# Kernel tuning notes

Hardware: AMD Instinct MI355X
Metric: run time of the kernel (lower is better)

Reference implementation:

```python
import jax, jax.numpy as jnp
import numpy as np

E, I, D = 8, 2816, 1024   # num_experts, intermediate_size, dim
T, A = 1024, 2            # tokens, top-k experts per token


def setup_inputs() -> dict:
    key = jax.random.key(0)
    k1, k2, k3, k4, k5 = jax.random.split(key, 5)
    x = jax.random.normal(k1, (T, D), dtype=jnp.float32)
    expert_indices = jax.random.randint(k2, (T, A), 0, E, dtype=jnp.int64)
    scale = 0.02
    w1 = jax.random.normal(k3, (E, I, D), dtype=jnp.float32) * scale
    w2 = jax.random.normal(k4, (E, D, I), dtype=jnp.float32) * scale
    w3 = jax.random.normal(k5, (E, I, D), dtype=jnp.float32) * scale
    return {"x": x, "w1": w1, "w2": w2, "w3": w3, "expert_indices": expert_indices}


def reference(x, w1, w2, w3, expert_indices):
    # x: [T, D], expert_indices: [T, A]
    # Same math as torch: silu(x @ w1[e].T) * (x @ w3[e].T) @ w2[e].T per (t, a).
    # Compute all-expert projections once, then gather the selected expert rows
    # (avoids materializing the [T, A, I, D] per-token weight copies).
    idx = expert_indices.astype(jnp.int32)
    h1 = jnp.einsum('ti,eoi->teo', x, w1)              # [T, E, I]
    h3 = jnp.einsum('ti,eoi->teo', x, w3)              # [T, E, I]
    g1 = jnp.take_along_axis(h1, idx[:, :, None], axis=1)  # [T, A, I]
    g3 = jnp.take_along_axis(h3, idx[:, :, None], axis=1)  # [T, A, I]
    h = jax.nn.silu(g1) * g3                            # SwiGLU, [T, A, I]
    y_all = jnp.einsum('tao,eio->taei', h, w2)          # [T, A, E, D]
    out = jnp.take_along_axis(y_all, idx[:, :, None, None], axis=2)  # [T, A, 1, D]
    return out[:, :, 0, :]                              # [T, A, D]
```

## Files before the change

kernel.cpp:

```cpp
#include <hip/hip_runtime.h>
#include <hip/hip_bf16.h>

#define E_NUM 8
#define I_DIM 2816
#define D_DIM 1024
#define T_NUM 1024
#define A_TOP 2
#define NPAIR (T_NUM * A_TOP)
#define PADROWS 3072
#define MT_MAX (PADROWS / 128)
#define KSPLIT 4
#define KCHUNK (I_DIM / KSPLIT)
#define KT2 (KCHUNK / 32)

#define HB_OFF    16384ULL
#define HB_BYTES  ((unsigned long long)PADROWS * I_DIM * 2ULL)
#define XBF_OFF   (HB_OFF + HB_BYTES)

typedef __bf16 bf16x8 __attribute__((ext_vector_type(8)));
typedef float  f32x4  __attribute__((ext_vector_type(4)));

__device__ inline unsigned pk2(float a, float b) {
  __hip_bfloat162 h = __float22bfloat162_rn(make_float2(a, b));
  union { __hip_bfloat162 h; unsigned u; } c; c.h = h; return c.u;
}
__device__ inline uint4 pack8(float4 a, float4 b) {
  return make_uint4(pk2(a.x, a.y), pk2(a.z, a.w), pk2(b.x, b.y), pk2(b.z, b.w));
}
__device__ inline unsigned short f2bf(float f) {
  __hip_bfloat16 h = __float2bfloat16(f);
  union { __hip_bfloat16 h; unsigned short u; } c; c.h = h; return c.u;
}
__device__ inline void gload_lds16(const unsigned short* g, unsigned short* l) {
  __builtin_amdgcn_global_load_lds((const __attribute__((address_space(1))) void*)g,
                                   (__attribute__((address_space(3))) void*)l, 16, 0, 0);
}

__global__ __launch_bounds__(256) void sort_pairs_kernel(
    const int* __restrict__ eidx, int* __restrict__ meta, int* __restrict__ pairs)
{
  __shared__ int cnt[E_NUM];
  __shared__ int pstart[E_NUM + 1];
  __shared__ int cur[E_NUM];
  int tid = threadIdx.x;
  if (tid < E_NUM) cnt[tid] = 0;
  __syncthreads();
  for (int p = tid; p < NPAIR; p += 256) atomicAdd(&cnt[eidx[p] & 7], 1);
  for (int i = tid; i < PADROWS; i += 256) pairs[i] = -1;
  __syncthreads();
  if (tid == 0) {
    int s = 0;
    for (int e = 0; e < E_NUM; ++e) {
      pstart[e] = s; cur[e] = s;
      s += ((cnt[e] + 127) / 128) * 128;
    }
    pstart[E_NUM] = s;
  }
  __syncthreads();
  for (int p = tid; p < NPAIR; p += 256) {
    int e = eidx[p] & 7;
    int pos = atomicAdd(&cur[e], 1);
    pairs[pos] = p;
  }
  __syncthreads();
  if (tid <= E_NUM) meta[tid] = pstart[tid];
}

__global__ __launch_bounds__(256) void convertx_kernel(
    const float* __restrict__ in, unsigned short* __restrict__ out)
{
  size_t i = (size_t)(blockIdx.x * 256 + threadIdx.x) * 8;
  const float4* p = (const float4*)(in + i);
  *(uint4*)(out + i) = pack8(p[0], p[1]);
}

__global__ __launch_bounds__(256, 4) void stage1_v5(
    const unsigned short* __restrict__ xbf, const float* __restrict__ w1,
    const float* __restrict__ w3, const int* __restrict__ meta,
    const int* __restrict__ pairs, unsigned short* __restrict__ hbuf)
{
  int mtile = blockIdx.y;
  if (mtile * 128 >= meta[E_NUM]) return;
  int e = 0;
  while (meta[e + 1] <= mtile * 128) ++e;
  int ntile = blockIdx.x;

  __shared__ alignas(16) unsigned short As[2][128 * 32];
  __shared__ alignas(16) unsigned short B1s[2][64 * 32];
  __shared__ alignas(16) unsigned short B3s[2][64 * 32];
  __shared__ int rowtok[128];

  int tid = threadIdx.x;
  for (int i = tid; i < 128; i += 256) {
    int p = pairs[mtile * 128 + i];
    rowtok[i] = (p >= 0) ? (p >> 1) : -1;
  }
  __syncthreads();

  int lane = tid & 63, w = tid >> 6;
  int wm = w >> 1, wn = w & 1, lrow = lane & 15, quad = lane >> 4;

  size_t axoff[2];
#pragma unroll
  for (int j = 0; j < 2; ++j) {
    int r = 32 * w + 16 * j + (lane >> 2);
    int tok = rowtok[r]; if (tok < 0) tok = 0;
    axoff[j] = (size_t)tok * D_DIM + (lane & 3) * 8;
  }
  const float* pw1 = w1 + ((size_t)e * I_DIM + ntile * 64 + (tid >> 2)) * D_DIM + (tid & 3) * 8;
  const float* pw3 = w3 + ((size_t)e * I_DIM + ntile * 64 + (tid >> 2)) * D_DIM + (tid & 3) * 8;
  int bws = (tid >> 2) * 32 + (tid & 3) * 8;

  f32x4 acc1[4][2], acc3[4][2];
#pragma unroll
  for (int i = 0; i < 4; ++i)
#pragma unroll
    for (int j = 0; j < 2; ++j) {
      acc1[i][j] = (f32x4){0.f, 0.f, 0.f, 0.f};
      acc3[i][j] = (f32x4){0.f, 0.f, 0.f, 0.f};
    }

  float4 r1[2], r3[2];
  r1[0] = *(const float4*)(pw1);     r1[1] = *(const float4*)(pw1 + 4);
  r3[0] = *(const float4*)(pw3);     r3[1] = *(const float4*)(pw3 + 4);
  gload_lds16(xbf + axoff[0], &As[0][(32 * w) * 32]);
  gload_lds16(xbf + axoff[1], &As[0][(32 * w + 16) * 32]);
  *(uint4*)&B1s[0][bws] = pack8(r1[0], r1[1]);
  *(uint4*)&B3s[0][bws] = pack8(r3[0], r3[1]);

  const int KT = D_DIM / 32;
  for (int k = 0; k < KT; ++k) {
    __syncthreads();
    int kk = k & 1;
    if (k + 1 < KT) {
      int kn = (k + 1) * 32;
      r1[0] = *(const float4*)(pw1 + kn); r1[1] = *(const float4*)(pw1 + kn + 4);
      r3[0] = *(const float4*)(pw3 + kn); r3[1] = *(const float4*)(pw3 + kn + 4);
      gload_lds16(xbf + axoff[0] + kn, &As[kk ^ 1][(32 * w) * 32]);
      gload_lds16(xbf + axoff[1] + kn, &As[kk ^ 1][(32 * w + 16) * 32]);
    }
    bf16x8 af[4];
#pragma unroll
    for (int mi = 0; mi < 4; ++mi)
      af[mi] = *(const bf16x8*)&As[kk][(wm * 64 + mi * 16 + lrow) * 32 + quad * 8];
#pragma unroll
    for (int ni = 0; ni < 2; ++ni) {
      bf16x8 b1 = *(const bf16x8*)&B1s[kk][(wn * 32 + ni * 16 + lrow) * 32 + quad * 8];
#pragma unroll
      for (int mi = 0; mi < 4; ++mi)
        acc1[mi][ni] = __builtin_amdgcn_mfma_f32_16x16x32_bf16(af[mi], b1, acc1[mi][ni], 0, 0, 0);
      bf16x8 b3 = *(const bf16x8*)&B3s[kk][(wn * 32 + ni * 16 + lrow) * 32 + quad * 8];
#pragma unroll
      for (int mi = 0; mi < 4; ++mi)
        acc3[mi][ni] = __builtin_amdgcn_mfma_f32_16x16x32_bf16(af[mi], b3, acc3[mi][ni], 0, 0, 0);
    }
    if (k + 1 < KT) {
      *(uint4*)&B1s[kk ^ 1][bws] = pack8(r1[0], r1[1]);
      *(uint4*)&B3s[kk ^ 1][bws] = pack8(r3[0], r3[1]);
    }
  }

#pragma unroll
  for (int mi = 0; mi < 4; ++mi) {
#pragma unroll
    for (int r = 0; r < 4; ++r) {
      int lr = wm * 64 + mi * 16 + quad * 4 + r;
      if (rowtok[lr] >= 0) {
        size_t base = (size_t)(mtile * 128 + lr) * I_DIM + (size_t)ntile * 64 + wn * 32;
#pragma unroll
        for (int ni = 0; ni < 2; ++ni) {
          float v1 = acc1[mi][ni][r];
          float v3 = acc3[mi][ni][r];
          float hv = (v1 / (1.f + __expf(-v1))) * v3;
          hbuf[base + ni * 16 + lrow] = f2bf(hv);
        }
      }
    }
  }
}

__global__ __launch_bounds__(256, 4) void stage2_v5(
    const unsigned short* __restrict__ hbuf, const float* __restrict__ w2,
    const int* __restrict__ meta, const int* __restrict__ pairs,
    float* __restrict__ out)
{
  int mtile = blockIdx.y;
  if (mtile * 128 >= meta[E_NUM]) return;
  int e = 0;
  while (meta[e + 1] <= mtile * 128) ++e;
  int ntile = blockIdx.x;
  int kbase = blockIdx.z * KCHUNK;

  __shared__ alignas(16) unsigned short As[2][128 * 32];
  __shared__ alignas(16) unsigned short Bs[2][128 * 32];
  __shared__ int prow[128];

  int tid = threadIdx.x;
  for (int i = tid; i < 128; i += 256) prow[i] = pairs[mtile * 128 + i];
  __syncthreads();

  int lane = tid & 63, w = tid >> 6;
  int wm = w >> 1, wn = w & 1, lrow = lane & 15, quad = lane >> 4;

  size_t axoff[2];
#pragma unroll
  for (int j = 0; j < 2; ++j) {
    int r = 32 * w + 16 * j + (lane >> 2);
    axoff[j] = (size_t)(mtile * 128 + r) * I_DIM + kbase + (lane & 3) * 8;
  }
  const float* pw2[2];
  int bws[2];
#pragma unroll
  for (int j = 0; j < 2; ++j) {
    int row = j * 64 + (tid >> 2);
    pw2[j] = w2 + ((size_t)e * D_DIM + ntile * 128 + row) * I_DIM + kbase + (tid & 3) * 8;
    bws[j] = row * 32 + (tid & 3) * 8;
  }

  f32x4 acc[4][4];
#pragma unroll
  for (int i = 0; i < 4; ++i)
#pragma unroll
    for (int j = 0; j < 4; ++j) acc[i][j] = (f32x4){0.f, 0.f, 0.f, 0.f};

  float4 rb[2][2];
#pragma unroll
  for (int j = 0; j < 2; ++j) {
    rb[j][0] = *(const float4*)(pw2[j]);
    rb[j][1] = *(const float4*)(pw2[j] + 4);
    gload_lds16(hbuf + axoff[j], &As[0][(32 * w + 16 * j) * 32]);
  }
#pragma unroll
  for (int j = 0; j < 2; ++j)
    *(uint4*)&Bs[0][bws[j]] = pack8(rb[j][0], rb[j][1]);

  for (int k = 0; k < KT2; ++k) {
    __syncthreads();
    int kk = k & 1;
    if (k + 1 < KT2) {
      int kn = (k + 1) * 32;
#pragma unroll
      for (int j = 0; j < 2; ++j) {
        rb[j][0] = *(const float4*)(pw2[j] + kn);
        rb[j][1] = *(const float4*)(pw2[j] + kn + 4);
        gload_lds16(hbuf + axoff[j] + kn, &As[kk ^ 1][(32 * w + 16 * j) * 32]);
      }
    }
    bf16x8 af[4];
#pragma unroll
    for (int mi = 0; mi < 4; ++mi)
      af[mi] = *(const bf16x8*)&As[kk][(wm * 64 + mi * 16 + lrow) * 32 + quad * 8];
#pragma unroll
    for (int ni = 0; ni < 4; ++ni) {
      bf16x8 bfr = *(const bf16x8*)&Bs[kk][(wn * 64 + ni * 16 + lrow) * 32 + quad * 8];
#pragma unroll
      for (int mi = 0; mi < 4; ++mi)
        acc[mi][ni] = __builtin_amdgcn_mfma_f32_16x16x32_bf16(af[mi], bfr, acc[mi][ni], 0, 0, 0);
    }
    if (k + 1 < KT2) {
#pragma unroll
      for (int j = 0; j < 2; ++j)
        *(uint4*)&Bs[kk ^ 1][bws[j]] = pack8(rb[j][0], rb[j][1]);
    }
  }

#pragma unroll
  for (int mi = 0; mi < 4; ++mi) {
#pragma unroll
    for (int r = 0; r < 4; ++r) {
      int lr = wm * 64 + mi * 16 + quad * 4 + r;
      int p = prow[lr];
      if (p >= 0) {
        float* obase = out + (size_t)p * D_DIM + (size_t)ntile * 128 + wn * 64;
#pragma unroll
        for (int ni = 0; ni < 4; ++ni)
          atomicAdd(obase + ni * 16 + lrow, acc[mi][ni][r]);
      }
    }
  }
}

extern "C" void kernel_launch(void* const* d_in, const int* in_sizes, int n_in,
                              void* d_out, int out_size, void* d_ws, size_t ws_size,
                              hipStream_t stream) {
  const float* x  = (const float*)d_in[0];
  const float* w1 = (const float*)d_in[1];
  const float* w2 = (const float*)d_in[2];
  const float* w3 = (const float*)d_in[3];
  const int* eidx = (const int*)d_in[4];
  float* out = (float*)d_out;

  int* meta  = (int*)d_ws;
  int* pairs = (int*)((char*)d_ws + 64);
  unsigned short* hbuf = (unsigned short*)((char*)d_ws + HB_OFF);
  unsigned short* xbf  = (unsigned short*)((char*)d_ws + XBF_OFF);

  sort_pairs_kernel<<<1, 256, 0, stream>>>(eidx, meta, pairs);
  convertx_kernel<<<(T_NUM * D_DIM) / 8 / 256, 256, 0, stream>>>(x, xbf);
  hipMemsetAsync(out, 0, (size_t)out_size * sizeof(float), stream);

  dim3 g1(I_DIM / 64, MT_MAX);
  stage1_v5<<<g1, 256, 0, stream>>>(xbf, w1, w3, meta, pairs, hbuf);
  dim3 g2(D_DIM / 128, MT_MAX, KSPLIT);
  stage2_v5<<<g2, 256, 0, stream>>>(hbuf, w2, meta, pairs, out);
}
```

Baseline: 337.5 us.

## Enlarge stage1 tile to 256x128 with 512 threads and XOR-swizzle LDS layouts

```diff
diff --git a/kernel.cpp b/kernel.cpp
--- a/kernel.cpp
+++ b/kernel.cpp
@@ -7,8 +7,9 @@
 #define T_NUM 1024
 #define A_TOP 2
 #define NPAIR (T_NUM * A_TOP)
-#define PADROWS 3072
-#define MT_MAX (PADROWS / 128)
+#define PADROWS 4096
+#define MT1 (PADROWS / 256)
+#define MT2 (PADROWS / 128)
 #define KSPLIT 4
 #define KCHUNK (I_DIM / KSPLIT)
 #define KT2 (KCHUNK / 32)
@@ -16,6 +17,8 @@
 #define HB_OFF    16384ULL
 #define HB_BYTES  ((unsigned long long)PADROWS * I_DIM * 2ULL)
 #define XBF_OFF   (HB_OFF + HB_BYTES)
+
+#define SW(r) (((r) ^ ((r) >> 2)) & 3)
 
 typedef __bf16 bf16x8 __attribute__((ext_vector_type(8)));
 typedef float  f32x4  __attribute__((ext_vector_type(4)));
@@ -52,7 +55,7 @@
     int s = 0;
     for (int e = 0; e < E_NUM; ++e) {
       pstart[e] = s; cur[e] = s;
-      s += ((cnt[e] + 127) / 128) * 128;
+      s += ((cnt[e] + 255) / 256) * 256;
     }
     pstart[E_NUM] = s;
   }
@@ -74,48 +77,45 @@
   *(uint4*)(out + i) = pack8(p[0], p[1]);
 }
 
-__global__ __launch_bounds__(256, 4) void stage1_v5(
+__global__ __launch_bounds__(512, 2) void stage1_v6(
     const unsigned short* __restrict__ xbf, const float* __restrict__ w1,
     const float* __restrict__ w3, const int* __restrict__ meta,
     const int* __restrict__ pairs, unsigned short* __restrict__ hbuf)
 {
   int mtile = blockIdx.y;
-  if (mtile * 128 >= meta[E_NUM]) return;
+  if (mtile * 256 >= meta[E_NUM]) return;
+  if (pairs[mtile * 256] < 0) return;
   int e = 0;
-  while (meta[e + 1] <= mtile * 128) ++e;
+  while (meta[e + 1] <= mtile * 256) ++e;
   int ntile = blockIdx.x;
 
-  __shared__ alignas(16) unsigned short As[2][128 * 32];
-  __shared__ alignas(16) unsigned short B1s[2][64 * 32];
-  __shared__ alignas(16) unsigned short B3s[2][64 * 32];
-  __shared__ int rowtok[128];
+  __shared__ alignas(16) unsigned short As[2][256 * 32];
+  __shared__ alignas(16) unsigned short B1s[2][128 * 32];
+  __shared__ alignas(16) unsigned short B3s[2][128 * 32];
 
   int tid = threadIdx.x;
-  for (int i = tid; i < 128; i += 256) {
-    int p = pairs[mtile * 128 + i];
-    rowtok[i] = (p >= 0) ? (p >> 1) : -1;
-  }
-  __syncthreads();
-
   int lane = tid & 63, w = tid >> 6;
   int wm = w >> 1, wn = w & 1, lrow = lane & 15, quad = lane >> 4;
-
-  size_t axoff[2];
+  int rq = (quad ^ SW(lrow)) * 8;
+
+  int axoff[2];
 #pragma unroll
   for (int j = 0; j < 2; ++j) {
     int r = 32 * w + 16 * j + (lane >> 2);
-    int tok = rowtok[r]; if (tok < 0) tok = 0;
-    axoff[j] = (size_t)tok * D_DIM + (lane & 3) * 8;
-  }
-  const float* pw1 = w1 + ((size_t)e * I_DIM + ntile * 64 + (tid >> 2)) * D_DIM + (tid & 3) * 8;
-  const float* pw3 = w3 + ((size_t)e * I_DIM + ntile * 64 + (tid >> 2)) * D_DIM + (tid & 3) * 8;
-  int bws = (tid >> 2) * 32 + (tid & 3) * 8;
-
-  f32x4 acc1[4][2], acc3[4][2];
+    int p = pairs[mtile * 256 + r];
+    int tok = (p >= 0) ? (p >> 1) : 0;
+    axoff[j] = tok * D_DIM + (((lane & 3) ^ SW(r)) * 8);
+  }
+  int brow = tid >> 2;
+  const float* pw1 = w1 + ((size_t)e * I_DIM + ntile * 128 + brow) * D_DIM + (tid & 3) * 8;
+  const float* pw3 = w3 + ((size_t)e * I_DIM + ntile * 128 + brow) * D_DIM + (tid & 3) * 8;
+  int bws = brow * 32 + (((tid & 3) ^ SW(brow)) * 8);
+
+  f32x4 acc1[4][4], acc3[4][4];
 #pragma unroll
   for (int i = 0; i < 4; ++i)
 #pragma unroll
-    for (int j = 0; j < 2; ++j) {
+    for (int j = 0; j < 4; ++j) {
       acc1[i][j] = (f32x4){0.f, 0.f, 0.f, 0.f};
       acc3[i][j] = (f32x4){0.f, 0.f, 0.f, 0.f};
     }
@@ -142,14 +142,14 @@
     bf16x8 af[4];
 #pragma unroll
     for (int mi = 0; mi < 4; ++mi)
-      af[mi] = *(const bf16x8*)&As[kk][(wm * 64 + mi * 16 + lrow) * 32 + quad * 8];
-#pragma unroll
-    for (int ni = 0; ni < 2; ++ni) {
-      bf16x8 b1 = *(const bf16x8*)&B1s[kk][(wn * 32 + ni * 16 + lrow) * 32 + quad * 8];
+      af[mi] = *(const bf16x8*)&As[kk][(wm * 64 + mi * 16 + lrow) * 32 + rq];
+#pragma unroll
+    for (int ni = 0; ni < 4; ++ni) {
+      bf16x8 b1 = *(const bf16x8*)&B1s[kk][(wn * 64 + ni * 16 + lrow) * 32 + rq];
 #pragma unroll
       for (int mi = 0; mi < 4; ++mi)
         acc1[mi][ni] = __builtin_amdgcn_mfma_f32_16x16x32_bf16(af[mi], b1, acc1[mi][ni], 0, 0, 0);
-      bf16x8 b3 = *(const bf16x8*)&B3s[kk][(wn * 32 + ni * 16 + lrow) * 32 + quad * 8];
+      bf16x8 b3 = *(const bf16x8*)&B3s[kk][(wn * 64 + ni * 16 + lrow) * 32 + rq];
 #pragma unroll
       for (int mi = 0; mi < 4; ++mi)
         acc3[mi][ni] = __builtin_amdgcn_mfma_f32_16x16x32_bf16(af[mi], b3, acc3[mi][ni], 0, 0, 0);
@@ -165,10 +165,11 @@
 #pragma unroll
     for (int r = 0; r < 4; ++r) {
       int lr = wm * 64 + mi * 16 + quad * 4 + r;
-      if (rowtok[lr] >= 0) {
-        size_t base = (size_t)(mtile * 128 + lr) * I_DIM + (size_t)ntile * 64 + wn * 32;
-#pragma unroll
-        for (int ni = 0; ni < 2; ++ni) {
+      int p = pairs[mtile * 256 + lr];
+      if (p >= 0) {
+        size_t base = (size_t)(mtile * 256 + lr) * I_DIM + (size_t)ntile * 128 + wn * 64;
+#pragma unroll
+        for (int ni = 0; ni < 4; ++ni) {
           float v1 = acc1[mi][ni][r];
           float v3 = acc3[mi][ni][r];
           float hv = (v1 / (1.f + __expf(-v1))) * v3;
@@ -179,13 +180,14 @@
   }
 }
 
-__global__ __launch_bounds__(256, 4) void stage2_v5(
+__global__ __launch_bounds__(256, 4) void stage2_v6(
     const unsigned short* __restrict__ hbuf, const float* __restrict__ w2,
     const int* __restrict__ meta, const int* __restrict__ pairs,
     float* __restrict__ out)
 {
   int mtile = blockIdx.y;
   if (mtile * 128 >= meta[E_NUM]) return;
+  if (pairs[mtile * 128] < 0) return;
   int e = 0;
   while (meta[e + 1] <= mtile * 128) ++e;
   int ntile = blockIdx.x;
@@ -201,12 +203,13 @@
 
   int lane = tid & 63, w = tid >> 6;
   int wm = w >> 1, wn = w & 1, lrow = lane & 15, quad = lane >> 4;
+  int rq = (quad ^ SW(lrow)) * 8;
 
   size_t axoff[2];
 #pragma unroll
   for (int j = 0; j < 2; ++j) {
     int r = 32 * w + 16 * j + (lane >> 2);
-    axoff[j] = (size_t)(mtile * 128 + r) * I_DIM + kbase + (lane & 3) * 8;
+    axoff[j] = (size_t)(mtile * 128 + r) * I_DIM + kbase + (((lane & 3) ^ SW(r)) * 8);
   }
   const float* pw2[2];
   int bws[2];
@@ -214,7 +217,7 @@
   for (int j = 0; j < 2; ++j) {
     int row = j * 64 + (tid >> 2);
     pw2[j] = w2 + ((size_t)e * D_DIM + ntile * 128 + row) * I_DIM + kbase + (tid & 3) * 8;
-    bws[j] = row * 32 + (tid & 3) * 8;
+    bws[j] = row * 32 + (((tid & 3) ^ SW(row)) * 8);
   }
 
   f32x4 acc[4][4];
@@ -249,10 +252,10 @@
     bf16x8 af[4];
 #pragma unroll
     for (int mi = 0; mi < 4; ++mi)
-      af[mi] = *(const bf16x8*)&As[kk][(wm * 64 + mi * 16 + lrow) * 32 + quad * 8];
+      af[mi] = *(const bf16x8*)&As[kk][(wm * 64 + mi * 16 + lrow) * 32 + rq];
 #pragma unroll
     for (int ni = 0; ni < 4; ++ni) {
-      bf16x8 bfr = *(const bf16x8*)&Bs[kk][(wn * 64 + ni * 16 + lrow) * 32 + quad * 8];
+      bf16x8 bfr = *(const bf16x8*)&Bs[kk][(wn * 64 + ni * 16 + lrow) * 32 + rq];
 #pragma unroll
       for (int mi = 0; mi < 4; ++mi)
         acc[mi][ni] = __builtin_amdgcn_mfma_f32_16x16x32_bf16(af[mi], bfr, acc[mi][ni], 0, 0, 0);
@@ -299,8 +302,8 @@
   convertx_kernel<<<(T_NUM * D_DIM) / 8 / 256, 256, 0, stream>>>(x, xbf);
   hipMemsetAsync(out, 0, (size_t)out_size * sizeof(float), stream);
 
-  dim3 g1(I_DIM / 64, MT_MAX);
-  stage1_v5<<<g1, 256, 0, stream>>>(xbf, w1, w3, meta, pairs, hbuf);
-  dim3 g2(D_DIM / 128, MT_MAX, KSPLIT);
-  stage2_v5<<<g2, 256, 0, stream>>>(hbuf, w2, meta, pairs, out);
-}
+  dim3 g1(I_DIM / 128, MT1);
+  stage1_v6<<<g1, 512, 0, stream>>>(xbf, w1, w3, meta, pairs, hbuf);
+  dim3 g2(D_DIM / 128, MT2, KSPLIT);
+  stage2_v6<<<g2, 256, 0, stream>>>(hbuf, w2, meta, pairs, out);
+}
```

Result: slower. 403.7 us (+19.6%).

## Double stage-1 M tile to 256 rows, fuse prep kernels, skip empty tiles

Applied to the files above, without the earlier changes.

```diff
diff --git a/kernel.cpp b/kernel.cpp
--- a/kernel.cpp
+++ b/kernel.cpp
@@ -7,8 +7,9 @@
 #define T_NUM 1024
 #define A_TOP 2
 #define NPAIR (T_NUM * A_TOP)
-#define PADROWS 3072
-#define MT_MAX (PADROWS / 128)
+#define PADROWS 4096
+#define MT1 (PADROWS / 256)
+#define MT2 (PADROWS / 128)
 #define KSPLIT 4
 #define KCHUNK (I_DIM / KSPLIT)
 #define KT2 (KCHUNK / 32)
@@ -36,80 +37,92 @@
                                    (__attribute__((address_space(3))) void*)l, 16, 0, 0);
 }
 
-__global__ __launch_bounds__(256) void sort_pairs_kernel(
-    const int* __restrict__ eidx, int* __restrict__ meta, int* __restrict__ pairs)
+__global__ __launch_bounds__(256) void prep_kernel(
+    const int* __restrict__ eidx, const float* __restrict__ x,
+    int* __restrict__ meta, int* __restrict__ pairs,
+    unsigned short* __restrict__ xbf, float* __restrict__ out)
 {
-  __shared__ int cnt[E_NUM];
-  __shared__ int pstart[E_NUM + 1];
-  __shared__ int cur[E_NUM];
+  int bid = blockIdx.x;
   int tid = threadIdx.x;
-  if (tid < E_NUM) cnt[tid] = 0;
-  __syncthreads();
-  for (int p = tid; p < NPAIR; p += 256) atomicAdd(&cnt[eidx[p] & 7], 1);
-  for (int i = tid; i < PADROWS; i += 256) pairs[i] = -1;
-  __syncthreads();
-  if (tid == 0) {
-    int s = 0;
-    for (int e = 0; e < E_NUM; ++e) {
-      pstart[e] = s; cur[e] = s;
-      s += ((cnt[e] + 127) / 128) * 128;
-    }
-    pstart[E_NUM] = s;
-  }
-  __syncthreads();
-  for (int p = tid; p < NPAIR; p += 256) {
-    int e = eidx[p] & 7;
-    int pos = atomicAdd(&cur[e], 1);
-    pairs[pos] = p;
-  }
-  __syncthreads();
-  if (tid <= E_NUM) meta[tid] = pstart[tid];
-}
-
-__global__ __launch_bounds__(256) void convertx_kernel(
-    const float* __restrict__ in, unsigned short* __restrict__ out)
-{
-  size_t i = (size_t)(blockIdx.x * 256 + threadIdx.x) * 8;
-  const float4* p = (const float4*)(in + i);
-  *(uint4*)(out + i) = pack8(p[0], p[1]);
-}
-
-__global__ __launch_bounds__(256, 4) void stage1_v5(
+  if (bid == 0) {
+    __shared__ int cnt[E_NUM];
+    __shared__ int pstart[E_NUM + 1];
+    __shared__ int cur[E_NUM];
+    if (tid < E_NUM) cnt[tid] = 0;
+    __syncthreads();
+    for (int p = tid; p < NPAIR; p += 256) atomicAdd(&cnt[eidx[p] & 7], 1);
+    for (int i = tid; i < PADROWS; i += 256) pairs[i] = -1;
+    __syncthreads();
+    if (tid == 0) {
+      int s = 0;
+      for (int e = 0; e < E_NUM; ++e) {
+        pstart[e] = s; cur[e] = s;
+        s += ((cnt[e] + 255) / 256) * 256;
+      }
+      pstart[E_NUM] = s;
+    }
+    __syncthreads();
+    for (int p = tid; p < NPAIR; p += 256) {
+      int e = eidx[p] & 7;
+      int pos = atomicAdd(&cur[e], 1);
+      pairs[pos] = p;
+    }
+    __syncthreads();
+    if (tid <= E_NUM) meta[tid] = pstart[tid];
+  } else if (bid <= 512) {
+    size_t i = (size_t)((bid - 1) * 256 + tid) * 8;
+    const float4* p = (const float4*)(x + i);
+    *(uint4*)(xbf + i) = pack8(p[0], p[1]);
+  } else {
+    uint4 z = make_uint4(0u, 0u, 0u, 0u);
+    uint4* po = (uint4*)out + (size_t)(bid - 513) * 1024 + tid;
+#pragma unroll
+    for (int k = 0; k < 4; ++k) po[k * 256] = z;
+  }
+}
+
+__global__ __launch_bounds__(512, 4) void stage1_v7(
     const unsigned short* __restrict__ xbf, const float* __restrict__ w1,
     const float* __restrict__ w3, const int* __restrict__ meta,
     const int* __restrict__ pairs, unsigned short* __restrict__ hbuf)
 {
   int mtile = blockIdx.y;
-  if (mtile * 128 >= meta[E_NUM]) return;
+  if (mtile * 256 >= meta[E_NUM]) return;
+  if (pairs[mtile * 256] < 0) return;
   int e = 0;
-  while (meta[e + 1] <= mtile * 128) ++e;
+  while (meta[e + 1] <= mtile * 256) ++e;
   int ntile = blockIdx.x;
 
-  __shared__ alignas(16) unsigned short As[2][128 * 32];
+  __shared__ alignas(16) unsigned short As[2][256 * 32];
   __shared__ alignas(16) unsigned short B1s[2][64 * 32];
   __shared__ alignas(16) unsigned short B3s[2][64 * 32];
-  __shared__ int rowtok[128];
+  __shared__ int prow[256];
 
   int tid = threadIdx.x;
-  for (int i = tid; i < 128; i += 256) {
-    int p = pairs[mtile * 128 + i];
-    rowtok[i] = (p >= 0) ? (p >> 1) : -1;
-  }
+  for (int i = tid; i < 256; i += 512) prow[i] = pairs[mtile * 256 + i];
   __syncthreads();
 
   int lane = tid & 63, w = tid >> 6;
-  int wm = w >> 1, wn = w & 1, lrow = lane & 15, quad = lane >> 4;
-
-  size_t axoff[2];
+  int wm = w >> 1, wn = w & 1;
+  int lrow = lane & 15, quad = lane >> 4;
+
+  int axoff[2];
 #pragma unroll
   for (int j = 0; j < 2; ++j) {
     int r = 32 * w + 16 * j + (lane >> 2);
-    int tok = rowtok[r]; if (tok < 0) tok = 0;
-    axoff[j] = (size_t)tok * D_DIM + (lane & 3) * 8;
-  }
-  const float* pw1 = w1 + ((size_t)e * I_DIM + ntile * 64 + (tid >> 2)) * D_DIM + (tid & 3) * 8;
-  const float* pw3 = w3 + ((size_t)e * I_DIM + ntile * 64 + (tid >> 2)) * D_DIM + (tid & 3) * 8;
-  int bws = (tid >> 2) * 32 + (tid & 3) * 8;
+    int p = prow[r];
+    int tok = (p >= 0) ? (p >> 1) : 0;
+    axoff[j] = tok * D_DIM + (lane & 3) * 8;
+  }
+  int mat = tid >> 8;
+  int bt = tid & 255;
+  int brow = bt >> 2, bchunk = bt & 3;
+  const float* pw = (mat ? w3 : w1) +
+      ((size_t)e * I_DIM + ntile * 64 + brow) * D_DIM + bchunk * 8;
+  int bws = brow * 32 + bchunk * 8;
+  unsigned short* bls[2];
+  bls[0] = mat ? B3s[0] : B1s[0];
+  bls[1] = mat ? B3s[1] : B1s[1];
 
   f32x4 acc1[4][2], acc3[4][2];
 #pragma unroll
@@ -120,13 +133,12 @@
       acc3[i][j] = (f32x4){0.f, 0.f, 0.f, 0.f};
     }
 
-  float4 r1[2], r3[2];
-  r1[0] = *(const float4*)(pw1);     r1[1] = *(const float4*)(pw1 + 4);
-  r3[0] = *(const float4*)(pw3);     r3[1] = *(const float4*)(pw3 + 4);
+  float4 rb[2];
+  rb[0] = *(const float4*)(pw);
+  rb[1] = *(const float4*)(pw + 4);
   gload_lds16(xbf + axoff[0], &As[0][(32 * w) * 32]);
   gload_lds16(xbf + axoff[1], &As[0][(32 * w + 16) * 32]);
-  *(uint4*)&B1s[0][bws] = pack8(r1[0], r1[1]);
-  *(uint4*)&B3s[0][bws] = pack8(r3[0], r3[1]);
+  *(uint4*)&bls[0][bws] = pack8(rb[0], rb[1]);
 
   const int KT = D_DIM / 32;
   for (int k = 0; k < KT; ++k) {
@@ -134,8 +146,8 @@
     int kk = k & 1;
     if (k + 1 < KT) {
       int kn = (k + 1) * 32;
-      r1[0] = *(const float4*)(pw1 + kn); r1[1] = *(const float4*)(pw1 + kn + 4);
-      r3[0] = *(const float4*)(pw3 + kn); r3[1] = *(const float4*)(pw3 + kn + 4);
+      rb[0] = *(const float4*)(pw + kn);
+      rb[1] = *(const float4*)(pw + kn + 4);
       gload_lds16(xbf + axoff[0] + kn, &As[kk ^ 1][(32 * w) * 32]);
       gload_lds16(xbf + axoff[1] + kn, &As[kk ^ 1][(32 * w + 16) * 32]);
     }
@@ -155,8 +167,7 @@
         acc3[mi][ni] = __builtin_amdgcn_mfma_f32_16x16x32_bf16(af[mi], b3, acc3[mi][ni], 0, 0, 0);
     }
     if (k + 1 < KT) {
-      *(uint4*)&B1s[kk ^ 1][bws] = pack8(r1[0], r1[1]);
-      *(uint4*)&B3s[kk ^ 1][bws] = pack8(r3[0], r3[1]);
+      *(uint4*)&bls[kk ^ 1][bws] = pack8(rb[0], rb[1]);
     }
   }
 
@@ -165,8 +176,9 @@
 #pragma unroll
     for (int r = 0; r < 4; ++r) {
       int lr = wm * 64 + mi * 16 + quad * 4 + r;
-      if (rowtok[lr] >= 0) {
-        size_t base = (size_t)(mtile * 128 + lr) * I_DIM + (size_t)ntile * 64 + wn * 32;
+      int p = prow[lr];
+      if (p >= 0) {
+        size_t base = (size_t)(mtile * 256 + lr) * I_DIM + (size_t)ntile * 64 + wn * 32;
 #pragma unroll
         for (int ni = 0; ni < 2; ++ni) {
           float v1 = acc1[mi][ni][r];
@@ -179,13 +191,14 @@
   }
 }
 
-__global__ __launch_bounds__(256, 4) void stage2_v5(
+__global__ __launch_bounds__(256, 4) void stage2_v7(
     const unsigned short* __restrict__ hbuf, const float* __restrict__ w2,
     const int* __restrict__ meta, const int* __restrict__ pairs,
     float* __restrict__ out)
 {
   int mtile = blockIdx.y;
   if (mtile * 128 >= meta[E_NUM]) return;
+  if (pairs[mtile * 128] < 0) return;
   int e = 0;
   while (meta[e + 1] <= mtile * 128) ++e;
   int ntile = blockIdx.x;
@@ -295,12 +308,10 @@
   unsigned short* hbuf = (unsigned short*)((char*)d_ws + HB_OFF);
   unsigned short* xbf  = (unsigned short*)((char*)d_ws + XBF_OFF);
 
-  sort_pairs_kernel<<<1, 256, 0, stream>>>(eidx, meta, pairs);
-  convertx_kernel<<<(T_NUM * D_DIM) / 8 / 256, 256, 0, stream>>>(x, xbf);
-  hipMemsetAsync(out, 0, (size_t)out_size * sizeof(float), stream);
-
-  dim3 g1(I_DIM / 64, MT_MAX);
-  stage1_v5<<<g1, 256, 0, stream>>>(xbf, w1, w3, meta, pairs, hbuf);
-  dim3 g2(D_DIM / 128, MT_MAX, KSPLIT);
-  stage2_v5<<<g2, 256, 0, stream>>>(hbuf, w2, meta, pairs, out);
-}
+  prep_kernel<<<1025, 256, 0, stream>>>(eidx, x, meta, pairs, xbf, out);
+
+  dim3 g1(I_DIM / 64, MT1);
+  stage1_v7<<<g1, 512, 0, stream>>>(xbf, w1, w3, meta, pairs, hbuf);
+  dim3 g2(D_DIM / 128, MT2, KSPLIT);
+  stage2_v7<<<g2, 256, 0, stream>>>(hbuf, w2, meta, pairs, out);
+}
```

Result: slower. 387.0 us (+14.7%).
